# Kernel tuning notes

Hardware: AMD Instinct MI355X
Metric: run time of the kernel (lower is better)

## Reference

```python
import jax, jax.numpy as jnp
import numpy as np

B, T, D, H = 2, 2048, 2048, 16
HD = D // H  # head_dim = 128


def setup_inputs() -> dict:
    key = jax.random.key(0)
    ks = jax.random.split(key, 7)
    s = 1.0 / np.sqrt(D)
    return {
        "x": jax.random.normal(ks[0], (B, T, D), jnp.float32),
        "Wq": jax.random.normal(ks[1], (D, D), jnp.float32) * s,
        "Wk": jax.random.normal(ks[2], (D, D), jnp.float32) * s,
        "Wv": jax.random.normal(ks[3], (D, D), jnp.float32) * s,
        "Wo": jax.random.normal(ks[4], (D, D), jnp.float32) * s,
        "rope_cos": jax.random.uniform(ks[5], (T, HD), jnp.float32, -1.0, 1.0),
        "rope_sin": jax.random.uniform(ks[6], (T, HD), jnp.float32, -1.0, 1.0),
    }


def _rope(x, cos, sin):
    # x: [B,H,T,HD]; cos/sin: [T,HD] broadcast over batch/heads
    half = x.shape[-1] // 2
    lhs, rhs = x[..., :half], x[..., half:]
    rotated = jnp.concatenate((-rhs, lhs), axis=-1)
    return cos[None, None] * x + rotated * sin[None, None]


def reference(x, Wq, Wk, Wv, Wo, rope_cos, rope_sin):
    Bc, Tc, Dc = x.shape
    # torch nn.Linear: y = x @ W.T
    q = (x @ Wq.T).reshape(Bc, Tc, H, HD).transpose(0, 2, 1, 3)
    k = (x @ Wk.T).reshape(Bc, Tc, H, HD).transpose(0, 2, 1, 3)
    v = (x @ Wv.T).reshape(Bc, Tc, H, HD).transpose(0, 2, 1, 3)
    q = _rope(q, rope_cos[:Tc], rope_sin[:Tc])
    k = _rope(k, rope_cos[:Tc], rope_sin[:Tc])
    scores = jnp.einsum('bhqd,bhkd->bhqk', q, k) / jnp.sqrt(jnp.float32(HD))
    causal = jnp.triu(jnp.ones((Tc, Tc), bool), k=1)
    scores = jnp.where(causal[None, None], -jnp.inf, scores)
    attn = jax.nn.softmax(scores, axis=-1)
    ctx = jnp.einsum('bhqk,bhkd->bhqd', attn, v)
    ctx = ctx.transpose(0, 2, 1, 3).reshape(Bc, Tc, Dc)
    return ctx @ Wo.T
```

## Files before the change

### kernel.cpp

```cpp
#include <hip/hip_runtime.h>

typedef __attribute__((ext_vector_type(4))) float   f32x4;
typedef __attribute__((ext_vector_type(8))) __bf16  bf16x8;
typedef __attribute__((ext_vector_type(4))) __bf16  bf16x4;
typedef __attribute__((ext_vector_type(8))) unsigned short u16x8;

#define NH   16
#define HD   128
#define TSEQ 2048
#define DM   2048
#define MT   4096

__device__ __forceinline__ f32x4 mfma_bf16(bf16x8 a, bf16x8 b, f32x4 c) {
  return __builtin_amdgcn_mfma_f32_16x16x32_bf16(a, b, c, 0, 0, 0);
}

__device__ __forceinline__ void gl_lds16(const __bf16* g, __bf16* l) {
  __builtin_amdgcn_global_load_lds(
      (const __attribute__((address_space(1))) void*)g,
      (__attribute__((address_space(3))) void*)l, 16, 0, 0);
}

__global__ __launch_bounds__(256) void k_cvtw(
    const float* __restrict__ X,
    const float* __restrict__ W0, const float* __restrict__ W1,
    const float* __restrict__ W2, const float* __restrict__ W3,
    __bf16* __restrict__ DX,
    __bf16* __restrict__ D0, __bf16* __restrict__ D1,
    __bf16* __restrict__ D2, __bf16* __restrict__ D3) {
  int z = blockIdx.z;
  const float* s = (z == 0) ? W0 : (z == 1) ? W1 : (z == 2) ? W2
                   : (z == 3) ? W3 : X;
  __bf16*      d = (z == 0) ? D0 : (z == 1) ? D1 : (z == 2) ? D2
                   : (z == 3) ? D3 : DX;
  int n4 = (z == 4) ? (MT * DM / 4) : (DM * DM / 4);
  int i = blockIdx.x * 256 + threadIdx.x;
  int stride = gridDim.x * 256;
  for (; i < n4; i += stride) {
    f32x4 v = ((const f32x4*)s)[i];
    bf16x4 o;
    o[0] = (__bf16)v[0]; o[1] = (__bf16)v[1];
    o[2] = (__bf16)v[2]; o[3] = (__bf16)v[3];
    ((bf16x4*)d)[i] = o;
  }
}

template <int MODE>
__global__ __launch_bounds__(256) void k_gemm(const __bf16* __restrict__ A,
                                              const __bf16* __restrict__ Bm,
                                              __bf16* __restrict__ Dst,
                                              float* __restrict__ F) {
  __shared__ __bf16 As[128 * 32];
  __shared__ __bf16 Bs[128 * 32];

  const int bid = blockIdx.x;
  const int wg  = (bid & 7) * 64 + (bid >> 3);
  const int n0  = (wg & 15) * 128;
  const int m0  = (wg >> 4) * 128;

  const int tid  = threadIdx.x;
  const int lane = tid & 63, w = tid >> 6;
  const int g    = lane >> 4, li = lane & 15;
  const int wr   = w >> 1, wc = w & 1;
  const int srow = lane >> 2;
  const int sseg = lane & 3;

  const f32x4 zero = {0.f, 0.f, 0.f, 0.f};
  f32x4 acc[4][4];
#pragma unroll
  for (int i = 0; i < 4; i++)
#pragma unroll
    for (int j = 0; j < 4; j++) acc[i][j] = zero;

  for (int k0 = 0; k0 < DM; k0 += 32) {
#pragma unroll
    for (int c = 0; c < 2; c++) {
      const int ch = w * 2 + c;
      gl_lds16(&A[(size_t)(m0 + ch * 16 + srow) * DM + k0 + sseg * 8],
               &As[ch * 512]);
      gl_lds16(&Bm[(size_t)(n0 + ch * 16 + srow) * DM + k0 + sseg * 8],
               &Bs[ch * 512]);
    }
    __syncthreads();
    bf16x8 af[4], bfr[4];
#pragma unroll
    for (int i = 0; i < 4; i++)
      af[i] = *(const bf16x8*)&As[(wr * 64 + i * 16 + li) * 32 + g * 8];
#pragma unroll
    for (int i = 0; i < 4; i++)
      bfr[i] = *(const bf16x8*)&Bs[(wc * 64 + i * 16 + li) * 32 + g * 8];
#pragma unroll
    for (int mi = 0; mi < 4; mi++)
#pragma unroll
      for (int ni = 0; ni < 4; ni++)
        acc[mi][ni] = mfma_bf16(af[mi], bfr[ni], acc[mi][ni]);
    __syncthreads();
  }

#pragma unroll
  for (int mi = 0; mi < 4; mi++)
#pragma unroll
    for (int ni = 0; ni < 4; ni++) {
      int colb = n0 + wc * 64 + ni * 16 + li;
#pragma unroll
      for (int r = 0; r < 4; r++) {
        int rowb = m0 + wr * 64 + mi * 16 + g * 4 + r;
        float vv = acc[mi][ni][r];
        if (MODE == 0) {
          F[(size_t)rowb * DM + colb] = vv;
        } else {
          int h = colb >> 7, d = colb & 127;
          int b = rowb >> 11, t = rowb & 2047;
          Dst[(((size_t)(b * NH + h)) * TSEQ + t) * HD + d] = (__bf16)vv;
        }
      }
    }
}

__global__ __launch_bounds__(256) void k_rope(__bf16* __restrict__ q,
                                              __bf16* __restrict__ kk,
                                              const float* __restrict__ rc,
                                              const float* __restrict__ rs) {
  int gid    = blockIdx.x * 256 + threadIdx.x;
  int tensor = gid >> 20;
  int rem    = gid & ((1 << 20) - 1);
  int bh     = rem >> 15;
  int r2     = rem & 32767;
  int t      = r2 >> 4;
  int j      = r2 & 15;
  int d0     = j * 4;
  __bf16* base = (tensor ? kk : q) + ((size_t)bh * TSEQ + t) * HD;
  f32x4 ca = *(const f32x4*)&rc[t * HD + d0];
  f32x4 cb = *(const f32x4*)&rc[t * HD + d0 + 64];
  f32x4 sa = *(const f32x4*)&rs[t * HD + d0];
  f32x4 sb = *(const f32x4*)&rs[t * HD + d0 + 64];
  bf16x4 xa = *(bf16x4*)&base[d0];
  bf16x4 xb = *(bf16x4*)&base[d0 + 64];
  bf16x4 oa, ob;
#pragma unroll
  for (int u = 0; u < 4; u++) {
    float fa = (float)xa[u], fb = (float)xb[u];
    oa[u] = (__bf16)(ca[u] * fa - fb * sa[u]);
    ob[u] = (__bf16)(cb[u] * fb + fa * sb[u]);
  }
  *(bf16x4*)&base[d0]      = oa;
  *(bf16x4*)&base[d0 + 64] = ob;
}

__global__ __launch_bounds__(256) void k_trans(const __bf16* __restrict__ v,
                                               __bf16* __restrict__ vt) {
  __shared__ unsigned short tile[64][73];
  int bh = blockIdx.z;
  int t0 = blockIdx.x * 64, d0 = blockIdx.y * 64;
  int tid = threadIdx.x;
  int r = tid >> 2, s4 = tid & 3;
  const unsigned short* src =
      (const unsigned short*)v + ((size_t)bh * TSEQ + t0) * HD + d0;
  u16x8 a = *(const u16x8*)&src[(size_t)r * HD + s4 * 16];
  u16x8 b = *(const u16x8*)&src[(size_t)r * HD + s4 * 16 + 8];
#pragma unroll
  for (int u = 0; u < 8; u++) {
    tile[r][s4 * 16 + u]     = a[u];
    tile[r][s4 * 16 + 8 + u] = b[u];
  }
  __syncthreads();
  unsigned short* dst =
      (unsigned short*)vt + ((size_t)bh * HD + d0) * TSEQ + t0;
  u16x8 o1, o2;
#pragma unroll
  for (int u = 0; u < 8; u++) {
    o1[u] = tile[s4 * 16 + u][r];
    o2[u] = tile[s4 * 16 + 8 + u][r];
  }
  *(u16x8*)&dst[(size_t)r * TSEQ + s4 * 16]     = o1;
  *(u16x8*)&dst[(size_t)r * TSEQ + s4 * 16 + 8] = o2;
}

__global__ __launch_bounds__(256, 2) void k_attn(const __bf16* __restrict__ q,
                                                 const __bf16* __restrict__ k,
                                                 const __bf16* __restrict__ vt,
                                                 __bf16* __restrict__ ctx) {
  __shared__ __bf16 Ks[64 * 136];
  __shared__ __bf16 Vs[128 * 72];
  __shared__ __bf16 Ps[4][32 * 72];

  const int bid = blockIdx.x;
  const int wg  = (bid & 7) * 64 + (bid >> 3);
  const int bh  = wg >> 4;
  const int qt  = 15 - (wg & 15);
  const int q0  = qt * 128;

  const int tid  = threadIdx.x;
  const int lane = tid & 63, w = tid >> 6;
  const int g    = lane >> 4, li = lane & 15;
  const int qw   = q0 + w * 32;

  const __bf16* qb = q  + (size_t)bh * TSEQ * HD;
  const __bf16* kb = k  + (size_t)bh * TSEQ * HD;
  const __bf16* vb = vt + (size_t)bh * HD * TSEQ;

  const float CST = 0.08838834764831845f * 1.4426950408889634f;
  bf16x8 qf[2][4];
#pragma unroll
  for (int s = 0; s < 2; s++)
#pragma unroll
    for (int kc = 0; kc < 4; kc++) {
      bf16x8 t =
          *(const bf16x8*)&qb[(size_t)(qw + s * 16 + li) * HD + kc * 32 + g * 8];
      bf16x8 o;
#pragma unroll
      for (int e = 0; e < 8; e++) o[e] = (__bf16)((float)t[e] * CST);
      qf[s][kc] = o;
    }

  const f32x4 zero = {0.f, 0.f, 0.f, 0.f};
  f32x4 o[2][8];
#pragma unroll
  for (int s = 0; s < 2; s++)
#pragma unroll
    for (int dt = 0; dt < 8; dt++) o[s][dt] = zero;
  float mrow[2] = {-1e30f, -1e30f};
  float lrow[2] = {0.f, 0.f};

  const int nkt = 2 * qt + 2;

  const int kR = tid >> 4, kS = tid & 15;
  const int vR = tid >> 3, vS = tid & 7;

  bf16x8 pk[4], pv[4];
#pragma unroll
  for (int i = 0; i < 4; i++) {
    pk[i] = *(const bf16x8*)&kb[(size_t)(kR + 16 * i) * HD + kS * 8];
    pv[i] = *(const bf16x8*)&vb[(size_t)(vR + 32 * i) * TSEQ + vS * 8];
  }

  for (int kt = 0; kt < nkt; kt++) {
    const int kv0 = kt * 64;
    __syncthreads();
#pragma unroll
    for (int i = 0; i < 4; i++)
      *(bf16x8*)&Ks[(kR + 16 * i) * 136 + kS * 8] = pk[i];
#pragma unroll
    for (int i = 0; i < 4; i++)
      *(bf16x8*)&Vs[(vR + 32 * i) * 72 + vS * 8] = pv[i];
    if (kt + 1 < nkt) {
      const int nv0 = kv0 + 64;
#pragma unroll
      for (int i = 0; i < 4; i++) {
        pk[i] = *(const bf16x8*)&kb[(size_t)(nv0 + kR + 16 * i) * HD + kS * 8];
        pv[i] = *(const bf16x8*)&vb[(size_t)(vR + 32 * i) * TSEQ + nv0 + vS * 8];
      }
    }
    __syncthreads();

    if (kv0 <= qw + 31) {
      f32x4 sc[2][4];
#pragma unroll
      for (int s = 0; s < 2; s++)
#pragma unroll
        for (int kvf = 0; kvf < 4; kvf++) sc[s][kvf] = zero;
#pragma unroll
      for (int kvf = 0; kvf < 4; kvf++)
#pragma unroll
        for (int kc = 0; kc < 4; kc++) {
          bf16x8 kf =
              *(const bf16x8*)&Ks[(kvf * 16 + li) * 136 + kc * 32 + g * 8];
          sc[0][kvf] = mfma_bf16(kf, qf[0][kc], sc[0][kvf]);
          sc[1][kvf] = mfma_bf16(kf, qf[1][kc], sc[1][kvf]);
        }
      if (kv0 + 63 > qw) {
#pragma unroll
        for (int s = 0; s < 2; s++) {
          const int qg = qw + s * 16 + li;
#pragma unroll
          for (int kvf = 0; kvf < 4; kvf++) {
#pragma unroll
            for (int r = 0; r < 4; r++) {
              int kg = kv0 + kvf * 16 + g * 4 + r;
              if (kg > qg) sc[s][kvf][r] = -1e30f;
            }
          }
        }
      }
      float mnew[2];
      bool upd = false;
#pragma unroll
      for (int s = 0; s < 2; s++) {
        float a = fmaxf(fmaxf(sc[s][0][0], sc[s][0][1]),
                        fmaxf(sc[s][0][2], sc[s][0][3]));
#pragma unroll
        for (int kvf = 1; kvf < 4; kvf++) {
          float b0 = fmaxf(sc[s][kvf][0], sc[s][kvf][1]);
          float b1 = fmaxf(sc[s][kvf][2], sc[s][kvf][3]);
          a = fmaxf(a, fmaxf(b0, b1));
        }
        a = fmaxf(a, __shfl_xor(a, 16));
        a = fmaxf(a, __shfl_xor(a, 32));
        mnew[s] = fmaxf(mrow[s], a);
        upd = upd || (a > mrow[s]);
      }
      if (__any(upd)) {
#pragma unroll
        for (int s = 0; s < 2; s++) {
          float fc = __builtin_amdgcn_exp2f(mrow[s] - mnew[s]);
          mrow[s] = mnew[s];
          lrow[s] *= fc;
#pragma unroll
          for (int r = 0; r < 4; r++) {
            float fr = __shfl(fc, (lane & 48) | (g * 4 + r));
#pragma unroll
            for (int dt = 0; dt < 8; dt++) o[s][dt][r] *= fr;
          }
        }
      }
#pragma unroll
      for (int s = 0; s < 2; s++) {
#pragma unroll
        for (int kvf = 0; kvf < 4; kvf++) {
          bf16x4 pk4;
#pragma unroll
          for (int r = 0; r < 4; r++) {
            float p = __builtin_amdgcn_exp2f(sc[s][kvf][r] - mrow[s]);
            lrow[s] += p;
            pk4[r] = (__bf16)p;
          }
          *(bf16x4*)&Ps[w][(s * 16 + li) * 72 + kvf * 16 + g * 4] = pk4;
        }
      }
      bf16x8 pa[2][2];
#pragma unroll
      for (int s = 0; s < 2; s++)
#pragma unroll
        for (int kvs = 0; kvs < 2; kvs++)
          pa[s][kvs] =
              *(const bf16x8*)&Ps[w][(s * 16 + li) * 72 + kvs * 32 + g * 8];
#pragma unroll
      for (int dt = 0; dt < 8; dt++) {
        bf16x8 v0 = *(const bf16x8*)&Vs[(dt * 16 + li) * 72 + g * 8];
        bf16x8 v1 = *(const bf16x8*)&Vs[(dt * 16 + li) * 72 + 32 + g * 8];
        o[0][dt] = mfma_bf16(pa[0][0], v0, o[0][dt]);
        o[0][dt] = mfma_bf16(pa[0][1], v1, o[0][dt]);
        o[1][dt] = mfma_bf16(pa[1][0], v0, o[1][dt]);
        o[1][dt] = mfma_bf16(pa[1][1], v1, o[1][dt]);
      }
    }
  }

  const int b = bh >> 4, h = bh & 15;
#pragma unroll
  for (int s = 0; s < 2; s++) {
    float l = lrow[s];
    l += __shfl_xor(l, 16);
    l += __shfl_xor(l, 32);
    float inv = 1.0f / l;
#pragma unroll
    for (int r = 0; r < 4; r++) {
      float ir = __shfl(inv, (lane & 48) | (g * 4 + r));
      size_t rowoff =
          ((size_t)(b * TSEQ + qw + s * 16 + g * 4 + r)) * DM + h * HD;
#pragma unroll
      for (int dt = 0; dt < 8; dt++)
        ctx[rowoff + dt * 16 + li] = (__bf16)(o[s][dt][r] * ir);
    }
  }
}

extern "C" void kernel_launch(void* const* d_in, const int* in_sizes, int n_in,
                              void* d_out, int out_size, void* d_ws,
                              size_t ws_size, hipStream_t stream) {
  const float* x  = (const float*)d_in[0];
  const float* Wq = (const float*)d_in[1];
  const float* Wk = (const float*)d_in[2];
  const float* Wv = (const float*)d_in[3];
  const float* Wo = (const float*)d_in[4];
  const float* rc = (const float*)d_in[5];
  const float* rs = (const float*)d_in[6];
  float* out = (float*)d_out;

  __bf16* xb   = (__bf16*)d_ws;
  __bf16* wqb  = xb  + (size_t)MT * DM;
  __bf16* wkb  = wqb + (size_t)DM * DM;
  __bf16* wvb  = wkb + (size_t)DM * DM;
  __bf16* wob  = wvb + (size_t)DM * DM;
  __bf16* qbuf = wob + (size_t)DM * DM;
  __bf16* kbuf = qbuf + (size_t)MT * DM;
  __bf16* vbuf = kbuf + (size_t)MT * DM;
  __bf16* vtb  = vbuf + (size_t)MT * DM;
  __bf16* ctxb = vbuf;

  dim3 gw(1024, 1, 5);
  k_cvtw<<<gw, 256, 0, stream>>>(x, Wq, Wk, Wv, Wo, xb, wqb, wkb, wvb, wob);

  k_gemm<1><<<512, 256, 0, stream>>>(xb, wqb, qbuf, nullptr);
  k_gemm<1><<<512, 256, 0, stream>>>(xb, wkb, kbuf, nullptr);
  k_gemm<1><<<512, 256, 0, stream>>>(xb, wvb, vbuf, nullptr);

  k_rope<<<8192, 256, 0, stream>>>(qbuf, kbuf, rc, rs);

  dim3 gt(TSEQ / 64, HD / 64, 32);
  k_trans<<<gt, 256, 0, stream>>>(vbuf, vtb);

  k_attn<<<512, 256, 0, stream>>>(qbuf, kbuf, vtb, ctxb);

  k_gemm<0><<<512, 256, 0, stream>>>(ctxb, wob, nullptr, out);
}
```

Baseline: 435.7 us.

## Fuse RoPE into Q/K projection epilogue and pair causal q-tiles per attention block

Adds a GEMM variant whose B-tile row mapping places dims d and d+64 in the same thread, so RoPE is applied in the epilogue and the standalone RoPE kernel's read-modify-write pass is removed. The attention kernel now launches half as many blocks, each processing a heavy and a light causal q-tile in sequence to balance work across CUs. The trade-off is that occupancy drops to one block per CU, and the fused epilogue does scattered scalar loads of cos/sin.

```diff
diff --git a/kernel.cpp b/kernel.cpp
--- a/kernel.cpp
+++ b/kernel.cpp
@@ -117,34 +117,80 @@
     }
 }
 
-__global__ __launch_bounds__(256) void k_rope(__bf16* __restrict__ q,
-                                              __bf16* __restrict__ kk,
-                                              const float* __restrict__ rc,
-                                              const float* __restrict__ rs) {
-  int gid    = blockIdx.x * 256 + threadIdx.x;
-  int tensor = gid >> 20;
-  int rem    = gid & ((1 << 20) - 1);
-  int bh     = rem >> 15;
-  int r2     = rem & 32767;
-  int t      = r2 >> 4;
-  int j      = r2 & 15;
-  int d0     = j * 4;
-  __bf16* base = (tensor ? kk : q) + ((size_t)bh * TSEQ + t) * HD;
-  f32x4 ca = *(const f32x4*)&rc[t * HD + d0];
-  f32x4 cb = *(const f32x4*)&rc[t * HD + d0 + 64];
-  f32x4 sa = *(const f32x4*)&rs[t * HD + d0];
-  f32x4 sb = *(const f32x4*)&rs[t * HD + d0 + 64];
-  bf16x4 xa = *(bf16x4*)&base[d0];
-  bf16x4 xb = *(bf16x4*)&base[d0 + 64];
-  bf16x4 oa, ob;
-#pragma unroll
-  for (int u = 0; u < 4; u++) {
-    float fa = (float)xa[u], fb = (float)xb[u];
-    oa[u] = (__bf16)(ca[u] * fa - fb * sa[u]);
-    ob[u] = (__bf16)(cb[u] * fb + fa * sb[u]);
-  }
-  *(bf16x4*)&base[d0]      = oa;
-  *(bf16x4*)&base[d0 + 64] = ob;
+__global__ __launch_bounds__(256) void k_gemm_rope(
+    const __bf16* __restrict__ A, const __bf16* __restrict__ Bm,
+    __bf16* __restrict__ Dst,
+    const float* __restrict__ rc, const float* __restrict__ rs) {
+  __shared__ __bf16 As[128 * 32];
+  __shared__ __bf16 Bs[128 * 32];
+
+  const int bid = blockIdx.x;
+  const int wg  = (bid & 7) * 64 + (bid >> 3);
+  const int n0  = (wg & 15) * 128;
+  const int m0  = (wg >> 4) * 128;
+
+  const int tid  = threadIdx.x;
+  const int lane = tid & 63, w = tid >> 6;
+  const int g    = lane >> 4, li = lane & 15;
+  const int wr   = w >> 1, wc = w & 1;
+  const int srow = lane >> 2;
+  const int sseg = lane & 3;
+
+  const f32x4 zero = {0.f, 0.f, 0.f, 0.f};
+  f32x4 acc[4][4];
+#pragma unroll
+  for (int i = 0; i < 4; i++)
+#pragma unroll
+    for (int j = 0; j < 4; j++) acc[i][j] = zero;
+
+  for (int k0 = 0; k0 < DM; k0 += 32) {
+#pragma unroll
+    for (int c = 0; c < 2; c++) {
+      const int ch = w * 2 + c;
+      gl_lds16(&A[(size_t)(m0 + ch * 16 + srow) * DM + k0 + sseg * 8],
+               &As[ch * 512]);
+      gl_lds16(&Bm[(size_t)(n0 + ch * 16 + srow) * DM + k0 + sseg * 8],
+               &Bs[ch * 512]);
+    }
+    __syncthreads();
+    bf16x8 af[4], bfr[4];
+#pragma unroll
+    for (int i = 0; i < 4; i++)
+      af[i] = *(const bf16x8*)&As[(wr * 64 + i * 16 + li) * 32 + g * 8];
+#pragma unroll
+    for (int i = 0; i < 4; i++)
+      bfr[i] = *(const bf16x8*)&Bs[(i * 32 + wc * 16 + li) * 32 + g * 8];
+#pragma unroll
+    for (int mi = 0; mi < 4; mi++)
+#pragma unroll
+      for (int ni = 0; ni < 4; ni++)
+        acc[mi][ni] = mfma_bf16(af[mi], bfr[ni], acc[mi][ni]);
+    __syncthreads();
+  }
+
+  const int h = n0 >> 7;
+  const int dl = wc * 16 + li;
+#pragma unroll
+  for (int mi = 0; mi < 4; mi++) {
+#pragma unroll
+    for (int r = 0; r < 4; r++) {
+      const int rowb = m0 + wr * 64 + mi * 16 + g * 4 + r;
+      const int b = rowb >> 11, t = rowb & 2047;
+      const float* rcb = rc + t * HD;
+      const float* rsb = rs + t * HD;
+      __bf16* outb = Dst + (((size_t)(b * NH + h)) * TSEQ + t) * HD;
+#pragma unroll
+      for (int ni = 0; ni < 2; ni++) {
+        const int d = ni * 32 + dl;
+        const float vlo = acc[mi][ni][r];
+        const float vhi = acc[mi][ni + 2][r];
+        const float clo = rcb[d],      slo = rsb[d];
+        const float chi = rcb[d + 64], shi = rsb[d + 64];
+        outb[d]      = (__bf16)(clo * vlo - slo * vhi);
+        outb[d + 64] = (__bf16)(chi * vhi + shi * vlo);
+      }
+    }
+  }
 }
 
 __global__ __launch_bounds__(256) void k_trans(const __bf16* __restrict__ v,
@@ -185,182 +231,187 @@
   __shared__ __bf16 Ps[4][32 * 72];
 
   const int bid = blockIdx.x;
-  const int wg  = (bid & 7) * 64 + (bid >> 3);
-  const int bh  = wg >> 4;
-  const int qt  = 15 - (wg & 15);
-  const int q0  = qt * 128;
+  const int wg  = (bid & 7) * 32 + (bid >> 3);
+  const int bh  = wg >> 3;
+  const int pi  = wg & 7;
 
   const int tid  = threadIdx.x;
   const int lane = tid & 63, w = tid >> 6;
   const int g    = lane >> 4, li = lane & 15;
-  const int qw   = q0 + w * 32;
 
   const __bf16* qb = q  + (size_t)bh * TSEQ * HD;
   const __bf16* kb = k  + (size_t)bh * TSEQ * HD;
   const __bf16* vb = vt + (size_t)bh * HD * TSEQ;
 
   const float CST = 0.08838834764831845f * 1.4426950408889634f;
-  bf16x8 qf[2][4];
-#pragma unroll
-  for (int s = 0; s < 2; s++)
-#pragma unroll
-    for (int kc = 0; kc < 4; kc++) {
-      bf16x8 t =
-          *(const bf16x8*)&qb[(size_t)(qw + s * 16 + li) * HD + kc * 32 + g * 8];
-      bf16x8 o;
-#pragma unroll
-      for (int e = 0; e < 8; e++) o[e] = (__bf16)((float)t[e] * CST);
-      qf[s][kc] = o;
-    }
-
   const f32x4 zero = {0.f, 0.f, 0.f, 0.f};
-  f32x4 o[2][8];
-#pragma unroll
-  for (int s = 0; s < 2; s++)
-#pragma unroll
-    for (int dt = 0; dt < 8; dt++) o[s][dt] = zero;
-  float mrow[2] = {-1e30f, -1e30f};
-  float lrow[2] = {0.f, 0.f};
-
-  const int nkt = 2 * qt + 2;
+  const int b = bh >> 4, h = bh & 15;
 
   const int kR = tid >> 4, kS = tid & 15;
   const int vR = tid >> 3, vS = tid & 7;
 
-  bf16x8 pk[4], pv[4];
-#pragma unroll
-  for (int i = 0; i < 4; i++) {
-    pk[i] = *(const bf16x8*)&kb[(size_t)(kR + 16 * i) * HD + kS * 8];
-    pv[i] = *(const bf16x8*)&vb[(size_t)(vR + 32 * i) * TSEQ + vS * 8];
-  }
-
-  for (int kt = 0; kt < nkt; kt++) {
-    const int kv0 = kt * 64;
-    __syncthreads();
-#pragma unroll
-    for (int i = 0; i < 4; i++)
-      *(bf16x8*)&Ks[(kR + 16 * i) * 136 + kS * 8] = pk[i];
-#pragma unroll
-    for (int i = 0; i < 4; i++)
-      *(bf16x8*)&Vs[(vR + 32 * i) * 72 + vS * 8] = pv[i];
-    if (kt + 1 < nkt) {
-      const int nv0 = kv0 + 64;
-#pragma unroll
-      for (int i = 0; i < 4; i++) {
-        pk[i] = *(const bf16x8*)&kb[(size_t)(nv0 + kR + 16 * i) * HD + kS * 8];
-        pv[i] = *(const bf16x8*)&vb[(size_t)(vR + 32 * i) * TSEQ + nv0 + vS * 8];
-      }
-    }
-    __syncthreads();
-
-    if (kv0 <= qw + 31) {
-      f32x4 sc[2][4];
-#pragma unroll
-      for (int s = 0; s < 2; s++)
-#pragma unroll
-        for (int kvf = 0; kvf < 4; kvf++) sc[s][kvf] = zero;
-#pragma unroll
-      for (int kvf = 0; kvf < 4; kvf++)
-#pragma unroll
-        for (int kc = 0; kc < 4; kc++) {
-          bf16x8 kf =
-              *(const bf16x8*)&Ks[(kvf * 16 + li) * 136 + kc * 32 + g * 8];
-          sc[0][kvf] = mfma_bf16(kf, qf[0][kc], sc[0][kvf]);
-          sc[1][kvf] = mfma_bf16(kf, qf[1][kc], sc[1][kvf]);
-        }
-      if (kv0 + 63 > qw) {
-#pragma unroll
-        for (int s = 0; s < 2; s++) {
-          const int qg = qw + s * 16 + li;
-#pragma unroll
-          for (int kvf = 0; kvf < 4; kvf++) {
-#pragma unroll
-            for (int r = 0; r < 4; r++) {
-              int kg = kv0 + kvf * 16 + g * 4 + r;
-              if (kg > qg) sc[s][kvf][r] = -1e30f;
+  for (int ph = 0; ph < 2; ph++) {
+    const int qt = ph ? pi : (15 - pi);
+    const int q0 = qt * 128;
+    const int qw = q0 + w * 32;
+    const int nkt = 2 * qt + 2;
+
+    bf16x8 qf[2][4];
+#pragma unroll
+    for (int s = 0; s < 2; s++)
+#pragma unroll
+      for (int kc = 0; kc < 4; kc++) {
+        bf16x8 t = *(const bf16x8*)&qb[(size_t)(qw + s * 16 + li) * HD +
+                                       kc * 32 + g * 8];
+        bf16x8 o;
+#pragma unroll
+        for (int e = 0; e < 8; e++) o[e] = (__bf16)((float)t[e] * CST);
+        qf[s][kc] = o;
+      }
+
+    f32x4 o[2][8];
+#pragma unroll
+    for (int s = 0; s < 2; s++)
+#pragma unroll
+      for (int dt = 0; dt < 8; dt++) o[s][dt] = zero;
+    float mrow[2] = {-1e30f, -1e30f};
+    float lrow[2] = {0.f, 0.f};
+
+    bf16x8 pk[4], pv[4];
+#pragma unroll
+    for (int i = 0; i < 4; i++) {
+      pk[i] = *(const bf16x8*)&kb[(size_t)(kR + 16 * i) * HD + kS * 8];
+      pv[i] = *(const bf16x8*)&vb[(size_t)(vR + 32 * i) * TSEQ + vS * 8];
+    }
+
+    for (int kt = 0; kt < nkt; kt++) {
+      const int kv0 = kt * 64;
+      __syncthreads();
+#pragma unroll
+      for (int i = 0; i < 4; i++)
+        *(bf16x8*)&Ks[(kR + 16 * i) * 136 + kS * 8] = pk[i];
+#pragma unroll
+      for (int i = 0; i < 4; i++)
+        *(bf16x8*)&Vs[(vR + 32 * i) * 72 + vS * 8] = pv[i];
+      if (kt + 1 < nkt) {
+        const int nv0 = kv0 + 64;
+#pragma unroll
+        for (int i = 0; i < 4; i++) {
+          pk[i] = *(const bf16x8*)&kb[(size_t)(nv0 + kR + 16 * i) * HD + kS * 8];
+          pv[i] =
+              *(const bf16x8*)&vb[(size_t)(vR + 32 * i) * TSEQ + nv0 + vS * 8];
+        }
+      }
+      __syncthreads();
+
+      if (kv0 <= qw + 31) {
+        f32x4 sc[2][4];
+#pragma unroll
+        for (int s = 0; s < 2; s++)
+#pragma unroll
+          for (int kvf = 0; kvf < 4; kvf++) sc[s][kvf] = zero;
+#pragma unroll
+        for (int kvf = 0; kvf < 4; kvf++)
+#pragma unroll
+          for (int kc = 0; kc < 4; kc++) {
+            bf16x8 kf =
+                *(const bf16x8*)&Ks[(kvf * 16 + li) * 136 + kc * 32 + g * 8];
+            sc[0][kvf] = mfma_bf16(kf, qf[0][kc], sc[0][kvf]);
+            sc[1][kvf] = mfma_bf16(kf, qf[1][kc], sc[1][kvf]);
+          }
+        if (kv0 + 63 > qw) {
+#pragma unroll
+          for (int s = 0; s < 2; s++) {
+            const int qg = qw + s * 16 + li;
+#pragma unroll
+            for (int kvf = 0; kvf < 4; kvf++) {
+#pragma unroll
+              for (int r = 0; r < 4; r++) {
+                int kg = kv0 + kvf * 16 + g * 4 + r;
+                if (kg > qg) sc[s][kvf][r] = -1e30f;
+              }
             }
           }
         }
-      }
-      float mnew[2];
-      bool upd = false;
-#pragma unroll
-      for (int s = 0; s < 2; s++) {
-        float a = fmaxf(fmaxf(sc[s][0][0], sc[s][0][1]),
-                        fmaxf(sc[s][0][2], sc[s][0][3]));
-#pragma unroll
-        for (int kvf = 1; kvf < 4; kvf++) {
-          float b0 = fmaxf(sc[s][kvf][0], sc[s][kvf][1]);
-          float b1 = fmaxf(sc[s][kvf][2], sc[s][kvf][3]);
-          a = fmaxf(a, fmaxf(b0, b1));
-        }
-        a = fmaxf(a, __shfl_xor(a, 16));
-        a = fmaxf(a, __shfl_xor(a, 32));
-        mnew[s] = fmaxf(mrow[s], a);
-        upd = upd || (a > mrow[s]);
-      }
-      if (__any(upd)) {
+        float mnew[2];
+        bool upd = false;
 #pragma unroll
         for (int s = 0; s < 2; s++) {
-          float fc = __builtin_amdgcn_exp2f(mrow[s] - mnew[s]);
-          mrow[s] = mnew[s];
-          lrow[s] *= fc;
-#pragma unroll
-          for (int r = 0; r < 4; r++) {
-            float fr = __shfl(fc, (lane & 48) | (g * 4 + r));
-#pragma unroll
-            for (int dt = 0; dt < 8; dt++) o[s][dt][r] *= fr;
+          float a = fmaxf(fmaxf(sc[s][0][0], sc[s][0][1]),
+                          fmaxf(sc[s][0][2], sc[s][0][3]));
+#pragma unroll
+          for (int kvf = 1; kvf < 4; kvf++) {
+            float b0 = fmaxf(sc[s][kvf][0], sc[s][kvf][1]);
+            float b1 = fmaxf(sc[s][kvf][2], sc[s][kvf][3]);
+            a = fmaxf(a, fmaxf(b0, b1));
           }
-        }
-      }
-#pragma unroll
-      for (int s = 0; s < 2; s++) {
-#pragma unroll
-        for (int kvf = 0; kvf < 4; kvf++) {
-          bf16x4 pk4;
-#pragma unroll
-          for (int r = 0; r < 4; r++) {
-            float p = __builtin_amdgcn_exp2f(sc[s][kvf][r] - mrow[s]);
-            lrow[s] += p;
-            pk4[r] = (__bf16)p;
+          a = fmaxf(a, __shfl_xor(a, 16));
+          a = fmaxf(a, __shfl_xor(a, 32));
+          mnew[s] = fmaxf(mrow[s], a);
+          upd = upd || (a > mrow[s]);
+        }
+        if (__any(upd)) {
+#pragma unroll
+          for (int s = 0; s < 2; s++) {
+            float fc = __builtin_amdgcn_exp2f(mrow[s] - mnew[s]);
+            mrow[s] = mnew[s];
+            lrow[s] *= fc;
+#pragma unroll
+            for (int r = 0; r < 4; r++) {
+              float fr = __shfl(fc, (lane & 48) | (g * 4 + r));
+#pragma unroll
+              for (int dt = 0; dt < 8; dt++) o[s][dt][r] *= fr;
+            }
           }
-          *(bf16x4*)&Ps[w][(s * 16 + li) * 72 + kvf * 16 + g * 4] = pk4;
-        }
-      }
-      bf16x8 pa[2][2];
-#pragma unroll
-      for (int s = 0; s < 2; s++)
-#pragma unroll
-        for (int kvs = 0; kvs < 2; kvs++)
-          pa[s][kvs] =
-              *(const bf16x8*)&Ps[w][(s * 16 + li) * 72 + kvs * 32 + g * 8];
-#pragma unroll
-      for (int dt = 0; dt < 8; dt++) {
-        bf16x8 v0 = *(const bf16x8*)&Vs[(dt * 16 + li) * 72 + g * 8];
-        bf16x8 v1 = *(const bf16x8*)&Vs[(dt * 16 + li) * 72 + 32 + g * 8];
-        o[0][dt] = mfma_bf16(pa[0][0], v0, o[0][dt]);
-        o[0][dt] = mfma_bf16(pa[0][1], v1, o[0][dt]);
-        o[1][dt] = mfma_bf16(pa[1][0], v0, o[1][dt]);
-        o[1][dt] = mfma_bf16(pa[1][1], v1, o[1][dt]);
-      }
-    }
-  }
-
-  const int b = bh >> 4, h = bh & 15;
-#pragma unroll
-  for (int s = 0; s < 2; s++) {
-    float l = lrow[s];
-    l += __shfl_xor(l, 16);
-    l += __shfl_xor(l, 32);
-    float inv = 1.0f / l;
-#pragma unroll
-    for (int r = 0; r < 4; r++) {
-      float ir = __shfl(inv, (lane & 48) | (g * 4 + r));
-      size_t rowoff =
-          ((size_t)(b * TSEQ + qw + s * 16 + g * 4 + r)) * DM + h * HD;
-#pragma unroll
-      for (int dt = 0; dt < 8; dt++)
-        ctx[rowoff + dt * 16 + li] = (__bf16)(o[s][dt][r] * ir);
+        }
+#pragma unroll
+        for (int s = 0; s < 2; s++) {
+#pragma unroll
+          for (int kvf = 0; kvf < 4; kvf++) {
+            bf16x4 pk4;
+#pragma unroll
+            for (int r = 0; r < 4; r++) {
+              float p = __builtin_amdgcn_exp2f(sc[s][kvf][r] - mrow[s]);
+              lrow[s] += p;
+              pk4[r] = (__bf16)p;
+            }
+            *(bf16x4*)&Ps[w][(s * 16 + li) * 72 + kvf * 16 + g * 4] = pk4;
+          }
+        }
+        bf16x8 pa[2][2];
+#pragma unroll
+        for (int s = 0; s < 2; s++)
+#pragma unroll
+          for (int kvs = 0; kvs < 2; kvs++)
+            pa[s][kvs] =
+                *(const bf16x8*)&Ps[w][(s * 16 + li) * 72 + kvs * 32 + g * 8];
+#pragma unroll
+        for (int dt = 0; dt < 8; dt++) {
+          bf16x8 v0 = *(const bf16x8*)&Vs[(dt * 16 + li) * 72 + g * 8];
+          bf16x8 v1 = *(const bf16x8*)&Vs[(dt * 16 + li) * 72 + 32 + g * 8];
+          o[0][dt] = mfma_bf16(pa[0][0], v0, o[0][dt]);
+          o[0][dt] = mfma_bf16(pa[0][1], v1, o[0][dt]);
+          o[1][dt] = mfma_bf16(pa[1][0], v0, o[1][dt]);
+          o[1][dt] = mfma_bf16(pa[1][1], v1, o[1][dt]);
+        }
+      }
+    }
+
+#pragma unroll
+    for (int s = 0; s < 2; s++) {
+      float l = lrow[s];
+      l += __shfl_xor(l, 16);
+      l += __shfl_xor(l, 32);
+      float inv = 1.0f / l;
+#pragma unroll
+      for (int r = 0; r < 4; r++) {
+        float ir = __shfl(inv, (lane & 48) | (g * 4 + r));
+        size_t rowoff =
+            ((size_t)(b * TSEQ + qw + s * 16 + g * 4 + r)) * DM + h * HD;
+#pragma unroll
+        for (int dt = 0; dt < 8; dt++)
+          ctx[rowoff + dt * 16 + li] = (__bf16)(o[s][dt][r] * ir);
+      }
     }
   }
 }
@@ -391,16 +442,14 @@
   dim3 gw(1024, 1, 5);
   k_cvtw<<<gw, 256, 0, stream>>>(x, Wq, Wk, Wv, Wo, xb, wqb, wkb, wvb, wob);
 
-  k_gemm<1><<<512, 256, 0, stream>>>(xb, wqb, qbuf, nullptr);
-  k_gemm<1><<<512, 256, 0, stream>>>(xb, wkb, kbuf, nullptr);
+  k_gemm_rope<<<512, 256, 0, stream>>>(xb, wqb, qbuf, rc, rs);
+  k_gemm_rope<<<512, 256, 0, stream>>>(xb, wkb, kbuf, rc, rs);
   k_gemm<1><<<512, 256, 0, stream>>>(xb, wvb, vbuf, nullptr);
-
-  k_rope<<<8192, 256, 0, stream>>>(qbuf, kbuf, rc, rs);
 
   dim3 gt(TSEQ / 64, HD / 64, 32);
   k_trans<<<gt, 256, 0, stream>>>(vbuf, vtb);
 
-  k_attn<<<512, 256, 0, stream>>>(qbuf, kbuf, vtb, ctxb);
+  k_attn<<<256, 256, 0, stream>>>(qbuf, kbuf, vtb, ctxb);
 
   k_gemm<0><<<512, 256, 0, stream>>>(ctxb, wob, nullptr, out);
 }
```

Measured after the change: 414.3 us. -4.9%, faster.
